# Kernel tuning notes

Hardware: AMD Instinct MI355X
Metric: run time of the kernel (lower is better)

The kernel has to match this reference:

```python
import jax, jax.numpy as jnp
import numpy as np

B, S1, S2 = 4, 2048, 2048
IN1, IN2 = 512, 512
KD, VD, H = 64, 64, 8


def setup_inputs() -> dict:
    key = jax.random.key(0)
    ks = jax.random.split(key, 7)
    x1 = jax.random.normal(ks[0], (B, S1, IN1), dtype=jnp.float32)
    x2 = jax.random.normal(ks[1], (B, S2, IN2), dtype=jnp.float32)
    # nn.Linear weights stored as [out, in]; kaiming-uniform-ish scale
    Wq = jax.random.normal(ks[2], (KD * H, IN1), dtype=jnp.float32) * (1.0 / np.sqrt(IN1))
    Wk = jax.random.normal(ks[3], (KD * H, IN2), dtype=jnp.float32) * (1.0 / np.sqrt(IN2))
    Wv = jax.random.normal(ks[4], (VD * H, IN2), dtype=jnp.float32) * (1.0 / np.sqrt(IN2))
    Wo = jax.random.normal(ks[5], (IN1, VD * H), dtype=jnp.float32) * (1.0 / np.sqrt(VD * H))
    bo = jax.random.normal(ks[6], (IN1,), dtype=jnp.float32) * 0.01
    return {"x1": x1, "x2": x2, "Wq": Wq, "Wk": Wk, "Wv": Wv, "Wo": Wo, "bo": bo}


def reference(x1, x2, Wq, Wk, Wv, Wo, bo):
    b, s1, _ = x1.shape
    s2 = x2.shape[1]
    # projections -> [B, H, S, D]
    q = (x1 @ Wq.T).reshape(b, s1, H, KD).transpose(0, 2, 1, 3)
    k = (x2 @ Wk.T).reshape(b, s2, H, KD).transpose(0, 2, 1, 3)
    v = (x2 @ Wv.T).reshape(b, s2, H, VD).transpose(0, 2, 1, 3)
    # scores [B, H, S1, S2]
    attn = jnp.einsum('bhqd,bhkd->bhqk', q, k) / jnp.sqrt(jnp.float32(KD))
    attn = jax.nn.softmax(attn, axis=-1)
    out = jnp.einsum('bhqk,bhkd->bhqd', attn, v)  # [B, H, S1, VD]
    out = out.transpose(0, 2, 1, 3).reshape(b, s1, H * VD)
    return out @ Wo.T + bo
```

## Files before the change

kernel.cpp:

```cpp
#include <hip/hip_runtime.h>
#include <stdint.h>

typedef __bf16 bf16;
typedef __bf16 bf16x8 __attribute__((ext_vector_type(8)));
typedef __bf16 bf16x4 __attribute__((ext_vector_type(4)));
typedef float f32x4 __attribute__((ext_vector_type(4)));
typedef float f32x16 __attribute__((ext_vector_type(16)));
typedef uint32_t u32x4 __attribute__((ext_vector_type(4)));

#define MFMA16x16x32(A, B, C) __builtin_amdgcn_mfma_f32_16x16x32_bf16((A), (B), (C), 0, 0, 0)
#define MFMA32x32x16(A, B, C) __builtin_amdgcn_mfma_f32_32x32x16_bf16((A), (B), (C), 0, 0, 0)
#define SBAR() do { __builtin_amdgcn_s_barrier(); __builtin_amdgcn_sched_barrier(0); } while (0)

__device__ __forceinline__ void gload_lds16(const void* g, void* l) {
  __builtin_amdgcn_global_load_lds((const __attribute__((address_space(1))) void*)g,
                                   (__attribute__((address_space(3))) void*)l,
                                   16, 0, 0);
}

__device__ __forceinline__ float fexp2(float x) { return __builtin_amdgcn_exp2f(x); }

__device__ __forceinline__ uint32_t cvtpk(float a, float b) {
  uint32_t r;
  asm("v_cvt_pk_bf16_f32 %0, %1, %2" : "=v"(r) : "v"(a), "v"(b));
  return r;
}
__device__ __forceinline__ void plswap(uint32_t& a, uint32_t& b) {
  asm volatile("v_permlane32_swap_b32 %0, %1" : "+v"(a), "+v"(b));
}

__device__ __forceinline__ bf16x8 cvt8(float4 a, float4 b) {
  bf16x8 o;
  o[0] = (bf16)a.x; o[1] = (bf16)a.y; o[2] = (bf16)a.z; o[3] = (bf16)a.w;
  o[4] = (bf16)b.x; o[5] = (bf16)b.y; o[6] = (bf16)b.z; o[7] = (bf16)b.w;
  return o;
}

__global__ void cast_x(const float* __restrict__ x1, const float* __restrict__ x2,
                       bf16* __restrict__ out) {
  const size_t i = ((size_t)blockIdx.x * blockDim.x + threadIdx.x) * 8;
  const float* src = (i < 4194304) ? x1 + i : x2 + (i - 4194304);
  float4 a = *reinterpret_cast<const float4*>(src);
  float4 b = *reinterpret_cast<const float4*>(src + 4);
  *reinterpret_cast<bf16x8*>(out + i) = cvt8(a, b);
}

template <int MODE>
__global__ __launch_bounds__(256, 4) void proj_kernel(
    const bf16* __restrict__ A0, const bf16* __restrict__ A1,
    const float* __restrict__ W0, const float* __restrict__ W1,
    const float* __restrict__ W2, void* __restrict__ C0, void* __restrict__ C1,
    void* __restrict__ C2, const float* __restrict__ bias) {
  __shared__ bf16 As[3][128 * 32];
  __shared__ bf16 Bs[2][64 * 32];
  const int tid = threadIdx.x;
  const int w = tid >> 6, l = tid & 63;
  const int wr = w >> 1, wc = w & 1;
  const int lr = l & 15, lg = l >> 4;
  const int bm = blockIdx.x, bn = blockIdx.y;
  const int K = 512;

  int sel = 0, wn = bn;
  const bf16* A;
  const float* Bf;
  if constexpr (MODE == 0) {
    sel = bn >> 3;
    wn = bn & 7;
    A = (sel == 0) ? A0 : A1;
    Bf = ((sel == 0) ? W0 : (sel == 1) ? W1 : W2) + (size_t)wn * 64 * K;
  } else {
    A = A0;
    Bf = W0 + (size_t)bn * 64 * K;
  }

  const int c_row = l >> 2;
  const int c_s = l & 3;
  const int sw = (c_s ^ (c_row & 3)) * 8;

  float4 lb[2][2];
  auto issue_A = [&](int t, int bb) {
#pragma unroll
    for (int i = 0; i < 2; i++) {
      const int q = w + i * 4;
      gload_lds16(A + (size_t)(bm * 128 + q * 16 + c_row) * K + t * 32 + sw, &As[bb][q * 512]);
    }
  };
  auto issue_B = [&](int t, int s) {
    const float* pb = Bf + (size_t)(w * 16 + c_row) * K + t * 32 + c_s * 8;
    lb[s][0] = *reinterpret_cast<const float4*>(pb);
    lb[s][1] = *reinterpret_cast<const float4*>(pb + 4);
  };
  auto commit_B = [&](int s, int bb) {
    *reinterpret_cast<bf16x8*>(&Bs[bb][w * 512 + c_row * 32 + sw]) = cvt8(lb[s][0], lb[s][1]);
  };

  f32x4 acc[4][2] = {};
  const int swz = (lr & 3) * 8;

  issue_A(0, 0); issue_B(0, 0);
  issue_A(1, 1); issue_B(1, 1);
  asm volatile("s_waitcnt vmcnt(4)" ::: "memory");
  commit_B(0, 0);
  asm volatile("s_waitcnt lgkmcnt(0)" ::: "memory");
  SBAR();

  const int NT = 16;
  for (int t = 0; t < NT; t++) {
    if (t + 2 < NT) { issue_A(t + 2, (t + 2) % 3); issue_B(t + 2, t & 1); }

    bf16x8 a[4], b[2];
    const int cur = t % 3;
#pragma unroll
    for (int mi = 0; mi < 4; mi++)
      a[mi] = *reinterpret_cast<const bf16x8*>(
          &As[cur][(wr * 64 + mi * 16 + lr) * 32 + (lg * 8 ^ swz)]);
#pragma unroll
    for (int ni = 0; ni < 2; ni++)
      b[ni] = *reinterpret_cast<const bf16x8*>(
          &Bs[t & 1][(wc * 32 + ni * 16 + lr) * 32 + (lg * 8 ^ swz)]);
#pragma unroll
    for (int mi = 0; mi < 4; mi++)
#pragma unroll
      for (int ni = 0; ni < 2; ni++)
        acc[mi][ni] = MFMA16x16x32(a[mi], b[ni], acc[mi][ni]);

    if (t + 1 < NT) {
      if (t + 2 < NT) asm volatile("s_waitcnt vmcnt(4)" ::: "memory");
      else            asm volatile("s_waitcnt vmcnt(0)" ::: "memory");
      commit_B((t + 1) & 1, (t + 1) & 1);
      asm volatile("s_waitcnt lgkmcnt(0)" ::: "memory");
      SBAR();
    }
  }

#pragma unroll
  for (int mi = 0; mi < 4; mi++) {
    const int m0 = bm * 128 + wr * 64 + mi * 16 + lg * 4;
#pragma unroll
    for (int ni = 0; ni < 2; ni++) {
      const int n = wc * 32 + ni * 16 + lr;
      if constexpr (MODE == 0) {
        const int gn = wn * 64 + n;
        if (sel < 2) {
          bf16* dst = (bf16*)((sel == 0) ? C0 : C1);
          const float scale = (sel == 0) ? 0.18033688011112f : 1.0f;
#pragma unroll
          for (int r = 0; r < 4; r++) {
            const int m = m0 + r;
            size_t d = (size_t)((m >> 11) * 8 + (gn >> 6)) * 131072 + (size_t)(m & 2047) * 64 + (gn & 63);
            dst[d] = (bf16)(acc[mi][ni][r] * scale);
          }
        } else {
          bf16x4 pv;
#pragma unroll
          for (int r = 0; r < 4; r++) pv[r] = (bf16)acc[mi][ni][r];
          size_t base = ((size_t)(m0 >> 11) * 512 + gn) * 2048 + (m0 & 2047);
          *reinterpret_cast<bf16x4*>((bf16*)C2 + base) = pv;
        }
      } else {
        const int gn = bn * 64 + n;
        const float bv = bias[gn];
#pragma unroll
        for (int r = 0; r < 4; r++)
          ((float*)C0)[(size_t)(m0 + r) * 512 + gn] = acc[mi][ni][r] + bv;
      }
    }
  }
}

__global__ __launch_bounds__(256, 2) void attn_kernel(
    const bf16* __restrict__ Q, const bf16* __restrict__ Kk,
    const bf16* __restrict__ Vt, bf16* __restrict__ AO) {
  __shared__ bf16 Kb2[3][64 * 64];
  __shared__ bf16 Vb2[3][64 * 64];

  const int tid = threadIdx.x;
  const int w = tid >> 6, l = tid & 63;
  const int q32 = l & 31;
  const int h = l >> 5;

  const int lin = blockIdx.x;
  const int xcd = lin & 7;
  const int m = lin >> 3;
  const int bh = xcd * 4 + (m & 3);
  const int qb = m >> 2;
  const int b = bh >> 3, hd = bh & 7;

  const bf16* Qb = Q + (size_t)bh * 131072;
  const bf16* Kb = Kk + (size_t)bh * 131072;
  const bf16* Vb = Vt + (size_t)bh * 131072;

  const int q0 = qb * 128 + w * 32;

  bf16x8 qf[4];
#pragma unroll
  for (int ks = 0; ks < 4; ks++)
    qf[ks] = *reinterpret_cast<const bf16x8*>(
        Qb + (size_t)(q0 + q32) * 64 + ks * 16 + h * 8);

  const int crow = l >> 3;
  const int scol = ((l & 7) ^ crow) * 8;
  auto stage = [&](int kv0, int bb) {
#pragma unroll
    for (int i = 0; i < 2; i++) {
      const int ch = w * 2 + i;
      const int row = ch * 8 + crow;
      gload_lds16(Kb + (size_t)(kv0 + row) * 64 + scol, &Kb2[bb][ch * 512]);
      gload_lds16(Vb + (size_t)row * 2048 + kv0 + scol, &Vb2[bb][ch * 512]);
    }
  };

  f32x16 oacc[2] = {};
  float lsum = 0.f;
  const int l7 = l & 7;

  stage(0, 0);
  stage(64, 1);
  asm volatile("s_waitcnt vmcnt(4)" ::: "memory");
  SBAR();

  for (int t = 0; t < 32; t++) {
    const int cur = t % 3;
    if (t + 2 < 32) stage((t + 2) * 64, (t + 2) % 3);

#pragma unroll
    for (int rb = 0; rb < 2; rb++) {
      bf16x8 kb[4];
#pragma unroll
      for (int ks = 0; ks < 4; ks++)
        kb[ks] = *reinterpret_cast<const bf16x8*>(
            &Kb2[cur][(rb * 32 + q32) * 64 + (((ks * 2 + h) ^ l7) * 8)]);

      f32x16 st = {};
#pragma unroll
      for (int ks = 0; ks < 4; ks++)
        st = MFMA32x32x16(kb[ks], qf[ks], st);

      float e[16];
#pragma unroll
      for (int r = 0; r < 16; r++) {
        e[r] = fexp2(st[r]);
        lsum += e[r];
      }
      uint32_t Qp[8];
#pragma unroll
      for (int p = 0; p < 8; p++) Qp[p] = cvtpk(e[2 * p], e[2 * p + 1]);
      plswap(Qp[0], Qp[2]);
      plswap(Qp[1], Qp[3]);
      plswap(Qp[4], Qp[6]);
      plswap(Qp[5], Qp[7]);
      const bf16x8 pa0 = __builtin_bit_cast(bf16x8, (u32x4){Qp[0], Qp[1], Qp[2], Qp[3]});
      const bf16x8 pa1 = __builtin_bit_cast(bf16x8, (u32x4){Qp[4], Qp[5], Qp[6], Qp[7]});

#pragma unroll
      for (int kst = 0; kst < 2; kst++) {
        const bf16x8 pa = (kst == 0) ? pa0 : pa1;
#pragma unroll
        for (int db = 0; db < 2; db++) {
          bf16x8 vb = *reinterpret_cast<const bf16x8*>(
              &Vb2[cur][(db * 32 + q32) * 64 + (((rb * 4 + kst * 2 + h) ^ l7) * 8)]);
          oacc[db] = MFMA32x32x16(pa, vb, oacc[db]);
        }
      }
    }

    if (t < 30)       asm volatile("s_waitcnt vmcnt(4) lgkmcnt(0)" ::: "memory");
    else if (t == 30) asm volatile("s_waitcnt vmcnt(0) lgkmcnt(0)" ::: "memory");
    if (t < 31) SBAR();
  }

  lsum += __shfl_xor(lsum, 32);

  float inv[16];
#pragma unroll
  for (int r = 0; r < 16; r++) {
    const int qv = (r & 3) + 8 * (r >> 2) + 4 * h;
    inv[r] = 1.f / __shfl(lsum, qv);
  }
#pragma unroll
  for (int db = 0; db < 2; db++) {
#pragma unroll
    for (int r = 0; r < 16; r++) {
      const int qv = (r & 3) + 8 * (r >> 2) + 4 * h;
      AO[(size_t)(b * 2048 + q0 + qv) * 512 + hd * 64 + db * 32 + q32] =
          (bf16)(oacc[db][r] * inv[r]);
    }
  }
}

extern "C" void kernel_launch(void* const* d_in, const int* in_sizes, int n_in,
                              void* d_out, int out_size, void* d_ws, size_t ws_size,
                              hipStream_t stream) {
  (void)in_sizes; (void)n_in; (void)out_size; (void)ws_size;
  const float* x1 = (const float*)d_in[0];
  const float* x2 = (const float*)d_in[1];
  const float* Wq = (const float*)d_in[2];
  const float* Wk = (const float*)d_in[3];
  const float* Wv = (const float*)d_in[4];
  const float* Wo = (const float*)d_in[5];
  const float* bo = (const float*)d_in[6];

  uint8_t* ws = (uint8_t*)d_ws;
  bf16* x1b = (bf16*)(ws + 0);
  bf16* x2b = (bf16*)(ws + 8388608);
  bf16* AO  = (bf16*)(ws + 0);
  bf16* Qws = (bf16*)(ws + 16777216);
  bf16* Kws = (bf16*)(ws + 25165824);
  bf16* Vtw = (bf16*)(ws + 33554432);

  cast_x<<<4096, 256, 0, stream>>>(x1, x2, x1b);

  proj_kernel<0><<<dim3(64, 24), 256, 0, stream>>>(x1b, x2b, Wq, Wk, Wv, Qws, Kws, Vtw, nullptr);

  attn_kernel<<<512, 256, 0, stream>>>(Qws, Kws, Vtw, AO);

  proj_kernel<1><<<dim3(64, 8), 256, 0, stream>>>(AO, nullptr, Wo, nullptr, nullptr, d_out, nullptr, nullptr, bo);
}
```

Measured before the change: 103.1 us.

## Pre-cast weights to bf16, use 128x128 QKV tiles, split KV across attention waves

The cast kernel now also converts all four weight matrices to bf16 in one launch. A new QKV projection kernel uses 128x128 tiles with both operands loaded via direct global-to-LDS, triple-buffered. The attention kernel now uses 64-query blocks where wave pairs split each KV tile and merge their partial outputs and sums through LDS, with double buffering and higher occupancy. The goal is more parallelism and less per-block register conversion work, at the cost of an extra LDS reduction step and a shallower prefetch pipeline.

```diff
diff --git a/kernel.cpp b/kernel.cpp
--- a/kernel.cpp
+++ b/kernel.cpp
@@ -37,20 +37,115 @@
 }
 
 __global__ void cast_x(const float* __restrict__ x1, const float* __restrict__ x2,
+                       const float* __restrict__ Wq, const float* __restrict__ Wk,
+                       const float* __restrict__ Wv, const float* __restrict__ Wo,
                        bf16* __restrict__ out) {
   const size_t i = ((size_t)blockIdx.x * blockDim.x + threadIdx.x) * 8;
-  const float* src = (i < 4194304) ? x1 + i : x2 + (i - 4194304);
+  const float* src;
+  if      (i < 4194304u) src = x1 + i;
+  else if (i < 8388608u) src = x2 + (i - 4194304u);
+  else if (i < 8650752u) src = Wq + (i - 8388608u);
+  else if (i < 8912896u) src = Wk + (i - 8650752u);
+  else if (i < 9175040u) src = Wv + (i - 8912896u);
+  else                   src = Wo + (i - 9175040u);
   float4 a = *reinterpret_cast<const float4*>(src);
   float4 b = *reinterpret_cast<const float4*>(src + 4);
   *reinterpret_cast<bf16x8*>(out + i) = cvt8(a, b);
 }
 
-template <int MODE>
-__global__ __launch_bounds__(256, 4) void proj_kernel(
-    const bf16* __restrict__ A0, const bf16* __restrict__ A1,
-    const float* __restrict__ W0, const float* __restrict__ W1,
-    const float* __restrict__ W2, void* __restrict__ C0, void* __restrict__ C1,
-    void* __restrict__ C2, const float* __restrict__ bias) {
+__global__ __launch_bounds__(256, 3) void qkv128_kernel(
+    const bf16* __restrict__ x1b, const bf16* __restrict__ x2b,
+    const bf16* __restrict__ Wb, bf16* __restrict__ Qw,
+    bf16* __restrict__ Kw, bf16* __restrict__ Vtw) {
+  __shared__ bf16 As[3][128 * 32];
+  __shared__ bf16 Bs[3][128 * 32];
+  const int tid = threadIdx.x;
+  const int w = tid >> 6, l = tid & 63;
+  const int wr = w >> 1, wc = w & 1;
+  const int lr = l & 15, lg = l >> 4;
+  const int bm = blockIdx.x, bn = blockIdx.y;
+  const int K = 512;
+  const int sel = bn >> 2, wn = bn & 3;
+
+  const bf16* A = (sel == 0) ? x1b : x2b;
+  const bf16* B = Wb + (size_t)sel * 262144 + (size_t)wn * 128 * K;
+
+  const int c_row = l >> 2;
+  const int sw = ((l & 3) ^ (c_row & 3)) * 8;
+
+  auto stage = [&](int t, int bb) {
+#pragma unroll
+    for (int i = 0; i < 2; i++) {
+      const int q = w + i * 4;
+      gload_lds16(A + (size_t)(bm * 128 + q * 16 + c_row) * K + t * 32 + sw, &As[bb][q * 512]);
+      gload_lds16(B + (size_t)(q * 16 + c_row) * K + t * 32 + sw, &Bs[bb][q * 512]);
+    }
+  };
+
+  f32x4 acc[4][4] = {};
+  const int swz = (lr & 3) * 8;
+
+  stage(0, 0);
+  stage(1, 1);
+  asm volatile("s_waitcnt vmcnt(4)" ::: "memory");
+  SBAR();
+
+  const int NT = 16;
+  for (int t = 0; t < NT; t++) {
+    if (t + 2 < NT) stage(t + 2, (t + 2) % 3);
+    const int cur = t % 3;
+    bf16x8 a[4], b[4];
+#pragma unroll
+    for (int mi = 0; mi < 4; mi++)
+      a[mi] = *reinterpret_cast<const bf16x8*>(
+          &As[cur][(wr * 64 + mi * 16 + lr) * 32 + (lg * 8 ^ swz)]);
+#pragma unroll
+    for (int ni = 0; ni < 4; ni++)
+      b[ni] = *reinterpret_cast<const bf16x8*>(
+          &Bs[cur][(wc * 64 + ni * 16 + lr) * 32 + (lg * 8 ^ swz)]);
+#pragma unroll
+    for (int mi = 0; mi < 4; mi++)
+#pragma unroll
+      for (int ni = 0; ni < 4; ni++)
+        acc[mi][ni] = MFMA16x16x32(a[mi], b[ni], acc[mi][ni]);
+
+    if (t + 1 < NT) {
+      if (t + 2 < NT) asm volatile("s_waitcnt vmcnt(4)" ::: "memory");
+      else            asm volatile("s_waitcnt vmcnt(0)" ::: "memory");
+      asm volatile("s_waitcnt lgkmcnt(0)" ::: "memory");
+      SBAR();
+    }
+  }
+
+  const float scale = (sel == 0) ? 0.18033688011112f : 1.0f;
+#pragma unroll
+  for (int mi = 0; mi < 4; mi++) {
+    const int m0 = bm * 128 + wr * 64 + mi * 16 + lg * 4;
+#pragma unroll
+    for (int ni = 0; ni < 4; ni++) {
+      const int gn = wn * 128 + wc * 64 + ni * 16 + lr;
+      if (sel < 2) {
+        bf16* dst = (sel == 0) ? Qw : Kw;
+#pragma unroll
+        for (int r = 0; r < 4; r++) {
+          const int m = m0 + r;
+          size_t d = (size_t)((m >> 11) * 8 + (gn >> 6)) * 131072 + (size_t)(m & 2047) * 64 + (gn & 63);
+          dst[d] = (bf16)(acc[mi][ni][r] * scale);
+        }
+      } else {
+        bf16x4 pv;
+#pragma unroll
+        for (int r = 0; r < 4; r++) pv[r] = (bf16)acc[mi][ni][r];
+        size_t base = ((size_t)(m0 >> 11) * 512 + gn) * 2048 + (m0 & 2047);
+        *reinterpret_cast<bf16x4*>(Vtw + base) = pv;
+      }
+    }
+  }
+}
+
+__global__ __launch_bounds__(256, 4) void outproj_kernel(
+    const bf16* __restrict__ A0, const float* __restrict__ W0,
+    float* __restrict__ C0, const float* __restrict__ bias) {
   __shared__ bf16 As[3][128 * 32];
   __shared__ bf16 Bs[2][64 * 32];
   const int tid = threadIdx.x;
@@ -60,19 +155,7 @@
   const int bm = blockIdx.x, bn = blockIdx.y;
   const int K = 512;
 
-  int sel = 0, wn = bn;
-  const bf16* A;
-  const float* Bf;
-  if constexpr (MODE == 0) {
-    sel = bn >> 3;
-    wn = bn & 7;
-    A = (sel == 0) ? A0 : A1;
-    Bf = ((sel == 0) ? W0 : (sel == 1) ? W1 : W2) + (size_t)wn * 64 * K;
-  } else {
-    A = A0;
-    Bf = W0 + (size_t)bn * 64 * K;
-  }
-
+  const float* Bf = W0 + (size_t)bn * 64 * K;
   const int c_row = l >> 2;
   const int c_s = l & 3;
   const int sw = (c_s ^ (c_row & 3)) * 8;
@@ -82,7 +165,7 @@
 #pragma unroll
     for (int i = 0; i < 2; i++) {
       const int q = w + i * 4;
-      gload_lds16(A + (size_t)(bm * 128 + q * 16 + c_row) * K + t * 32 + sw, &As[bb][q * 512]);
+      gload_lds16(A0 + (size_t)(bm * 128 + q * 16 + c_row) * K + t * 32 + sw, &As[bb][q * 512]);
     }
   };
   auto issue_B = [&](int t, int s) {
@@ -138,46 +221,26 @@
     const int m0 = bm * 128 + wr * 64 + mi * 16 + lg * 4;
 #pragma unroll
     for (int ni = 0; ni < 2; ni++) {
-      const int n = wc * 32 + ni * 16 + lr;
-      if constexpr (MODE == 0) {
-        const int gn = wn * 64 + n;
-        if (sel < 2) {
-          bf16* dst = (bf16*)((sel == 0) ? C0 : C1);
-          const float scale = (sel == 0) ? 0.18033688011112f : 1.0f;
-#pragma unroll
-          for (int r = 0; r < 4; r++) {
-            const int m = m0 + r;
-            size_t d = (size_t)((m >> 11) * 8 + (gn >> 6)) * 131072 + (size_t)(m & 2047) * 64 + (gn & 63);
-            dst[d] = (bf16)(acc[mi][ni][r] * scale);
-          }
-        } else {
-          bf16x4 pv;
-#pragma unroll
-          for (int r = 0; r < 4; r++) pv[r] = (bf16)acc[mi][ni][r];
-          size_t base = ((size_t)(m0 >> 11) * 512 + gn) * 2048 + (m0 & 2047);
-          *reinterpret_cast<bf16x4*>((bf16*)C2 + base) = pv;
-        }
-      } else {
-        const int gn = bn * 64 + n;
-        const float bv = bias[gn];
-#pragma unroll
-        for (int r = 0; r < 4; r++)
-          ((float*)C0)[(size_t)(m0 + r) * 512 + gn] = acc[mi][ni][r] + bv;
-      }
-    }
-  }
-}
-
-__global__ __launch_bounds__(256, 2) void attn_kernel(
+      const int gn = bn * 64 + wc * 32 + ni * 16 + lr;
+      const float bv = bias[gn];
+#pragma unroll
+      for (int r = 0; r < 4; r++)
+        C0[(size_t)(m0 + r) * 512 + gn] = acc[mi][ni][r] + bv;
+    }
+  }
+}
+
+__global__ __launch_bounds__(256, 4) void attn_kernel(
     const bf16* __restrict__ Q, const bf16* __restrict__ Kk,
     const bf16* __restrict__ Vt, bf16* __restrict__ AO) {
-  __shared__ bf16 Kb2[3][64 * 64];
-  __shared__ bf16 Vb2[3][64 * 64];
+  __shared__ bf16 Kb2[2][64 * 64];
+  __shared__ bf16 Vb2[2][64 * 64];
 
   const int tid = threadIdx.x;
   const int w = tid >> 6, l = tid & 63;
   const int q32 = l & 31;
   const int h = l >> 5;
+  const int qg = w >> 1, kvh = w & 1;
 
   const int lin = blockIdx.x;
   const int xcd = lin & 7;
@@ -190,7 +253,7 @@
   const bf16* Kb = Kk + (size_t)bh * 131072;
   const bf16* Vb = Vt + (size_t)bh * 131072;
 
-  const int q0 = qb * 128 + w * 32;
+  const int q0 = qb * 64 + qg * 32;
 
   bf16x8 qf[4];
 #pragma unroll
@@ -215,75 +278,93 @@
   const int l7 = l & 7;
 
   stage(0, 0);
-  stage(64, 1);
-  asm volatile("s_waitcnt vmcnt(4)" ::: "memory");
+  asm volatile("s_waitcnt vmcnt(0)" ::: "memory");
   SBAR();
 
   for (int t = 0; t < 32; t++) {
-    const int cur = t % 3;
-    if (t + 2 < 32) stage((t + 2) * 64, (t + 2) % 3);
-
-#pragma unroll
-    for (int rb = 0; rb < 2; rb++) {
-      bf16x8 kb[4];
-#pragma unroll
-      for (int ks = 0; ks < 4; ks++)
-        kb[ks] = *reinterpret_cast<const bf16x8*>(
-            &Kb2[cur][(rb * 32 + q32) * 64 + (((ks * 2 + h) ^ l7) * 8)]);
-
-      f32x16 st = {};
-#pragma unroll
-      for (int ks = 0; ks < 4; ks++)
-        st = MFMA32x32x16(kb[ks], qf[ks], st);
-
-      float e[16];
-#pragma unroll
-      for (int r = 0; r < 16; r++) {
-        e[r] = fexp2(st[r]);
-        lsum += e[r];
+    const int cur = t & 1;
+    if (t < 31) stage((t + 1) * 64, cur ^ 1);
+
+    bf16x8 kb[4];
+#pragma unroll
+    for (int ks = 0; ks < 4; ks++)
+      kb[ks] = *reinterpret_cast<const bf16x8*>(
+          &Kb2[cur][(kvh * 32 + q32) * 64 + (((ks * 2 + h) ^ l7) * 8)]);
+
+    f32x16 st = {};
+#pragma unroll
+    for (int ks = 0; ks < 4; ks++)
+      st = MFMA32x32x16(kb[ks], qf[ks], st);
+
+    float e[16];
+#pragma unroll
+    for (int r = 0; r < 16; r++) {
+      e[r] = fexp2(st[r]);
+      lsum += e[r];
+    }
+    uint32_t Qp[8];
+#pragma unroll
+    for (int p = 0; p < 8; p++) Qp[p] = cvtpk(e[2 * p], e[2 * p + 1]);
+    plswap(Qp[0], Qp[2]);
+    plswap(Qp[1], Qp[3]);
+    plswap(Qp[4], Qp[6]);
+    plswap(Qp[5], Qp[7]);
+    const bf16x8 pa0 = __builtin_bit_cast(bf16x8, (u32x4){Qp[0], Qp[1], Qp[2], Qp[3]});
+    const bf16x8 pa1 = __builtin_bit_cast(bf16x8, (u32x4){Qp[4], Qp[5], Qp[6], Qp[7]});
+
+#pragma unroll
+    for (int kst = 0; kst < 2; kst++) {
+      const bf16x8 pa = (kst == 0) ? pa0 : pa1;
+#pragma unroll
+      for (int db = 0; db < 2; db++) {
+        bf16x8 vb = *reinterpret_cast<const bf16x8*>(
+            &Vb2[cur][(db * 32 + q32) * 64 + (((kvh * 4 + kst * 2 + h) ^ l7) * 8)]);
+        oacc[db] = MFMA32x32x16(pa, vb, oacc[db]);
       }
-      uint32_t Qp[8];
-#pragma unroll
-      for (int p = 0; p < 8; p++) Qp[p] = cvtpk(e[2 * p], e[2 * p + 1]);
-      plswap(Qp[0], Qp[2]);
-      plswap(Qp[1], Qp[3]);
-      plswap(Qp[4], Qp[6]);
-      plswap(Qp[5], Qp[7]);
-      const bf16x8 pa0 = __builtin_bit_cast(bf16x8, (u32x4){Qp[0], Qp[1], Qp[2], Qp[3]});
-      const bf16x8 pa1 = __builtin_bit_cast(bf16x8, (u32x4){Qp[4], Qp[5], Qp[6], Qp[7]});
-
-#pragma unroll
-      for (int kst = 0; kst < 2; kst++) {
-        const bf16x8 pa = (kst == 0) ? pa0 : pa1;
-#pragma unroll
-        for (int db = 0; db < 2; db++) {
-          bf16x8 vb = *reinterpret_cast<const bf16x8*>(
-              &Vb2[cur][(db * 32 + q32) * 64 + (((rb * 4 + kst * 2 + h) ^ l7) * 8)]);
-          oacc[db] = MFMA32x32x16(pa, vb, oacc[db]);
-        }
-      }
-    }
-
-    if (t < 30)       asm volatile("s_waitcnt vmcnt(4) lgkmcnt(0)" ::: "memory");
-    else if (t == 30) asm volatile("s_waitcnt vmcnt(0) lgkmcnt(0)" ::: "memory");
-    if (t < 31) SBAR();
+    }
+
+    if (t < 31) {
+      asm volatile("s_waitcnt vmcnt(0) lgkmcnt(0)" ::: "memory");
+      SBAR();
+    }
   }
 
   lsum += __shfl_xor(lsum, 32);
 
-  float inv[16];
-#pragma unroll
-  for (int r = 0; r < 16; r++) {
-    const int qv = (r & 3) + 8 * (r >> 2) + 4 * h;
-    inv[r] = 1.f / __shfl(lsum, qv);
-  }
-#pragma unroll
-  for (int db = 0; db < 2; db++) {
+  float* cb = (float*)&Kb2[0][0];
+  float* ls = (float*)&Vb2[0][0];
+  __syncthreads();
+  if (kvh == 1) {
+#pragma unroll
+    for (int db = 0; db < 2; db++)
+#pragma unroll
+      for (int r = 0; r < 16; r++)
+        cb[((qg * 2 + db) * 16 + r) * 64 + l] = oacc[db][r];
+    if (l < 32) ls[qg * 32 + q32] = lsum;
+  }
+  __syncthreads();
+  if (kvh == 0) {
+    lsum += ls[qg * 32 + q32];
+#pragma unroll
+    for (int db = 0; db < 2; db++)
+#pragma unroll
+      for (int r = 0; r < 16; r++)
+        oacc[db][r] += cb[((qg * 2 + db) * 16 + r) * 64 + l];
+
+    float inv[16];
 #pragma unroll
     for (int r = 0; r < 16; r++) {
       const int qv = (r & 3) + 8 * (r >> 2) + 4 * h;
-      AO[(size_t)(b * 2048 + q0 + qv) * 512 + hd * 64 + db * 32 + q32] =
-          (bf16)(oacc[db][r] * inv[r]);
+      inv[r] = 1.f / __shfl(lsum, qv);
+    }
+#pragma unroll
+    for (int db = 0; db < 2; db++) {
+#pragma unroll
+      for (int r = 0; r < 16; r++) {
+        const int qv = (r & 3) + 8 * (r >> 2) + 4 * h;
+        AO[(size_t)(b * 2048 + q0 + qv) * 512 + hd * 64 + db * 32 + q32] =
+            (bf16)(oacc[db][r] * inv[r]);
+      }
     }
   }
 }
@@ -303,16 +384,17 @@
   uint8_t* ws = (uint8_t*)d_ws;
   bf16* x1b = (bf16*)(ws + 0);
   bf16* x2b = (bf16*)(ws + 8388608);
+  bf16* Wsb = (bf16*)(ws + 16777216);
   bf16* AO  = (bf16*)(ws + 0);
-  bf16* Qws = (bf16*)(ws + 16777216);
-  bf16* Kws = (bf16*)(ws + 25165824);
-  bf16* Vtw = (bf16*)(ws + 33554432);
-
-  cast_x<<<4096, 256, 0, stream>>>(x1, x2, x1b);
-
-  proj_kernel<0><<<dim3(64, 24), 256, 0, stream>>>(x1b, x2b, Wq, Wk, Wv, Qws, Kws, Vtw, nullptr);
-
-  attn_kernel<<<512, 256, 0, stream>>>(Qws, Kws, Vtw, AO);
-
-  proj_kernel<1><<<dim3(64, 8), 256, 0, stream>>>(AO, nullptr, Wo, nullptr, nullptr, d_out, nullptr, nullptr, bo);
-}
+  bf16* Qws = (bf16*)(ws + 18874368);
+  bf16* Kws = (bf16*)(ws + 27262976);
+  bf16* Vtw = (bf16*)(ws + 35651584);
+
+  cast_x<<<4608, 256, 0, stream>>>(x1, x2, Wq, Wk, Wv, Wo, x1b);
+
+  qkv128_kernel<<<dim3(64, 12), 256, 0, stream>>>(x1b, x2b, Wsb, Qws, Kws, Vtw);
+
+  attn_kernel<<<1024, 256, 0, stream>>>(Qws, Kws, Vtw, AO);
+
+  outproj_kernel<<<dim3(64, 8), 256, 0, stream>>>(AO, Wo, (float*)d_out, bo);
+}
```

New measurement: 103.5 us. About the same (+0.4%).
